# Kernel tuning notes

Measured on AMD Instinct MI355X. Metric: run time of the kernel, lower is better.

Reference implementation:

```python
import jax, jax.numpy as jnp
import numpy as np

STATE_DIM, ACTION_DIM, HIDDEN_DIM = 512, 64, 2048
INPUT_DIM = STATE_DIM + ACTION_DIM + 1  # 577
BATCH = 4096


def setup_inputs() -> dict:
    key = jax.random.key(0)
    ks = jax.random.split(key, 12)
    sc_x = 1.0 / np.sqrt(INPUT_DIM)
    sc_h = 1.0 / np.sqrt(HIDDEN_DIM)
    return {
        "s": jax.random.normal(ks[0], (BATCH, STATE_DIM), jnp.float32),
        "a_prev": jax.random.normal(ks[1], (BATCH, ACTION_DIM), jnp.float32),
        "r_prev": jax.random.normal(ks[2], (BATCH, 1), jnp.float32),
        "h": jnp.zeros((HIDDEN_DIM,), jnp.float32),
        "c": jnp.zeros((HIDDEN_DIM,), jnp.float32),
        # Fused gate weights: columns ordered [i, f, g(c-tilde), o]
        "Wx": jax.random.uniform(ks[3], (INPUT_DIM, 4 * HIDDEN_DIM), jnp.float32, -sc_x, sc_x),
        "Wh": jax.random.uniform(ks[4], (HIDDEN_DIM, 4 * HIDDEN_DIM), jnp.float32, -sc_h, sc_h),
        "bh": jax.random.uniform(ks[5], (4 * HIDDEN_DIM,), jnp.float32, -sc_h, sc_h),
        "Wa": jax.random.uniform(ks[6], (HIDDEN_DIM, ACTION_DIM), jnp.float32, -sc_h, sc_h),
        "ba": jax.random.uniform(ks[7], (ACTION_DIM,), jnp.float32, -sc_h, sc_h),
        "Wv": jax.random.uniform(ks[8], (HIDDEN_DIM, 1), jnp.float32, -sc_h, sc_h),
        "bv": jax.random.uniform(ks[9], (1,), jnp.float32, -sc_h, sc_h),
    }


def reference(s, a_prev, r_prev, h, c, Wx, Wh, bh, Wa, ba, Wv, bv):
    # x: [B, input_dim]
    x = jnp.concatenate([s, a_prev, r_prev], axis=1)
    # Two fused GEMMs replace the 8 separate small linears (same math).
    z = x @ Wx + h @ Wh + bh          # [B, 4H]
    zi, zf, zg, zo = jnp.split(z, 4, axis=-1)
    i = jax.nn.sigmoid(zi)
    f = jax.nn.sigmoid(zf)
    c_new = f * c + i * jnp.tanh(zg)  # [B, H] (c broadcast over batch)
    o = jax.nn.sigmoid(zo)
    h_new = o * jnp.tanh(c_new)       # [B, H]
    probs = jax.nn.softmax(h_new @ Wa + ba, axis=1)  # [B, A]
    v = h_new @ Wv + bv               # [B, 1]
    return (probs, v)
```

## Files before the change

kernel.cpp:

```cpp
#include <hip/hip_runtime.h>
#include <hip/hip_bf16.h>

#define BATCH   4096
#define SDIM    512
#define ADIM    64
#define IDIM    577
#define KP2     576
#define NKT64   9
#define HDIM    2048
#define ZDIM    8192
#define BUFE    (128 * 64)

typedef __attribute__((ext_vector_type(8))) __bf16 bf16x8;
typedef __attribute__((ext_vector_type(4))) __bf16 bf16x4;
typedef __attribute__((ext_vector_type(4))) float  accx4;

__global__ __launch_bounds__(256) void setup_kernel(
    const float* __restrict__ s, const float* __restrict__ a_prev,
    const float* __restrict__ h,
    const float* __restrict__ wx, const float* __restrict__ wh,
    const float* __restrict__ wa,
    __hip_bfloat16* __restrict__ xb, __hip_bfloat16* __restrict__ wxt,
    __hip_bfloat16* __restrict__ waT, float* __restrict__ zh_w)
{
    __shared__ float stile[64 * 65];
    const int bid = blockIdx.x;
    const int t = threadIdx.x;

    if (bid < 1152) {
        const int kt2 = bid >> 7;
        const int nt  = bid & 127;
        const int c4  = t & 15;
        const int rr  = t >> 4;
#pragma unroll
        for (int i = 0; i < 4; ++i) {
            const int r = rr + i * 16;
            const int k = kt2 * 64 + r;
            float4 v =
                *(const float4*)(wx + (size_t)k * ZDIM + nt * 64 + c4 * 4);
            *(float4*)(stile + r * 65 + c4 * 4) = v;
        }
        __syncthreads();
        const int ch = t & 7;
#pragma unroll
        for (int i = 0; i < 2; ++i) {
            const int nr = (t >> 3) + i * 32;
            bf16x8 w8;
#pragma unroll
            for (int j = 0; j < 8; ++j)
                w8[j] = (__bf16)stile[(ch * 8 + j) * 65 + nr];
            *(bf16x8*)(wxt + (size_t)(nt * 64 + nr) * KP2 + kt2 * 64 + ch * 8)
                = w8;
        }
    } else if (bid < 2176) {
        const int zb = bid - 1152;
        const int nb = zb & 63, ky = zb >> 6;
        const int n  = nb * 128 + (t & 127);
        const int kh = t >> 7;
        const float* hp  = h + ky * 128 + kh * 64;
        const float* whp = wh + (size_t)(ky * 128 + kh * 64) * ZDIM + n;
        float p = 0.0f;
#pragma unroll 32
        for (int kk = 0; kk < 64; ++kk)
            p = fmaf(hp[kk], whp[(size_t)kk * ZDIM], p);
        stile[t] = p;
        __syncthreads();
        if (t < 128)
            zh_w[ky * ZDIM + n] = stile[t] + stile[t + 128];
    } else if (bid < 2432) {
        const int row0 = (bid - 2176) * 16;
        const int tr = t >> 4, tc = t & 15;
        const int row = row0 + tr;
        const float* srow = s + (size_t)row * SDIM;
        const float* arow = a_prev + (size_t)row * ADIM;
        __hip_bfloat16* xrow = xb + (size_t)row * KP2;
#pragma unroll
        for (int j = 0; j < 9; ++j) {
            const int c4  = j * 16 + tc;
            const int col = c4 * 4;
            float4 v = (col < SDIM)
                ? *(const float4*)(srow + col)
                : *(const float4*)(arow + (col - SDIM));
            bf16x4 w;
            w[0] = (__bf16)v.x; w[1] = (__bf16)v.y;
            w[2] = (__bf16)v.z; w[3] = (__bf16)v.w;
            *(bf16x4*)(xrow + col) = w;
        }
    } else {
        const int wb = bid - 2432;
        const int kt = wb >> 1, at = wb & 1;
        const int c  = t & 31, r0 = t >> 5;
#pragma unroll
        for (int i = 0; i < 4; ++i) {
            int r = r0 + i * 8;
            stile[r * 33 + c] = wa[(size_t)(kt * 32 + r) * ADIM + at * 32 + c];
        }
        __syncthreads();
#pragma unroll
        for (int i = 0; i < 4; ++i) {
            int r = r0 + i * 8;
            waT[(size_t)(at * 32 + r) * HDIM + kt * 32 + c] =
                __float2bfloat16(stile[c * 33 + r]);
        }
    }
}

__device__ __forceinline__ float rcp_f(float x) {
    return __builtin_amdgcn_rcpf(x);
}
__device__ __forceinline__ float sigmoid_f(float x) {
    return rcp_f(1.0f + __expf(-x));
}
__device__ __forceinline__ float tanh_f(float x) {
    return 1.0f - 2.0f * rcp_f(1.0f + __expf(2.0f * x));
}

__global__ __launch_bounds__(256, 4) void lstm_gemm(
    const __hip_bfloat16* __restrict__ xb,
    const __hip_bfloat16* __restrict__ wxt,
    const float* __restrict__ zh_w,
    const float* __restrict__ bh,
    const float* __restrict__ cvec,
    const float* __restrict__ wx,
    const float* __restrict__ r_prev,
    __hip_bfloat16* __restrict__ hout)
{
    __shared__ __bf16 smA[BUFE];
    __shared__ __bf16 smB[BUFE];
    const int t    = threadIdx.x;
    const int lane = t & 63;
    const int wid  = t >> 6;
    const int m0   = blockIdx.x * 128;
    const int n0   = blockIdx.y * 32;
    const int wm   = wid >> 1, wn = wid & 1;
    const int fl15 = lane & 15;
    const int fhi  = lane >> 4;

    accx4 acc[4][4] = {};

    const int srow = lane >> 3;
    const int slot = lane & 7;
    const int cch  = slot ^ srow;
    const __bf16* gA[4]; const __bf16* gB[4]; int lofs[4];
#pragma unroll
    for (int i = 0; i < 4; ++i) {
        const int r = wid * 32 + i * 8 + srow;
        gA[i] = (const __bf16*)xb + (size_t)(m0 + r) * KP2 + cch * 8;
        const int g = r >> 5, nn = r & 31;
        gB[i] = (const __bf16*)wxt +
                (size_t)(g * HDIM + n0 + nn) * KP2 + cch * 8;
        lofs[i] = (wid * 32 + i * 8) * 64;
    }

    auto stage = [&](int tile) {
        const int ko = tile * 64;
#pragma unroll
        for (int i = 0; i < 4; ++i) {
            __builtin_amdgcn_global_load_lds(
                (const __attribute__((address_space(1))) void*)(gA[i] + ko),
                (__attribute__((address_space(3))) void*)(smA + lofs[i]),
                16, 0, 0);
            __builtin_amdgcn_global_load_lds(
                (const __attribute__((address_space(1))) void*)(gB[i] + ko),
                (__attribute__((address_space(3))) void*)(smB + lofs[i]),
                16, 0, 0);
        }
    };

    auto compute = [&]() {
#pragma unroll
        for (int hf = 0; hf < 2; ++hf) {
            const int ck = hf * 4 + fhi;
            const int sl = (ck ^ (fl15 & 7)) * 8;
            bf16x8 af[4], bfr[4];
#pragma unroll
            for (int rt = 0; rt < 4; ++rt)
                af[rt] = *(const bf16x8*)(smA +
                    (wm * 64 + rt * 16 + fl15) * 64 + sl);
#pragma unroll
            for (int g = 0; g < 4; ++g)
                bfr[g] = *(const bf16x8*)(smB +
                    (g * 32 + wn * 16 + fl15) * 64 + sl);
#pragma unroll
            for (int g = 0; g < 4; ++g)
#pragma unroll
                for (int rt = 0; rt < 4; ++rt)
                    acc[g][rt] = __builtin_amdgcn_mfma_f32_16x16x32_bf16(
                        af[rt], bfr[g], acc[g][rt], 0, 0, 0);
        }
    };

#pragma unroll
    for (int kt = 0; kt < NKT64; ++kt) {
        if (kt) __syncthreads();
        stage(kt);
        __syncthreads();
        compute();
    }

    const int colg = n0 + wn * 16 + fl15;
    float zsum[4], wxr[4];
#pragma unroll
    for (int g = 0; g < 4; ++g) {
        float z = bh[g * HDIM + colg];
#pragma unroll
        for (int j = 0; j < 16; ++j)
            z += zh_w[j * ZDIM + g * HDIM + colg];
        zsum[g] = z;
        wxr[g] = wx[(size_t)576 * ZDIM + g * HDIM + colg];
    }
    const float cv = cvec[colg];
#pragma unroll
    for (int rt = 0; rt < 4; ++rt) {
#pragma unroll
        for (int r = 0; r < 4; ++r) {
            const int row = m0 + wm * 64 + rt * 16 + (fhi << 2) + r;
            const float rv = r_prev[row];
            const float zi = acc[0][rt][r] + zsum[0] + rv * wxr[0];
            const float zf = acc[1][rt][r] + zsum[1] + rv * wxr[1];
            const float zg = acc[2][rt][r] + zsum[2] + rv * wxr[2];
            const float zo = acc[3][rt][r] + zsum[3] + rv * wxr[3];
            const float cn = sigmoid_f(zf) * cv + sigmoid_f(zi) * tanh_f(zg);
            const float hn = sigmoid_f(zo) * tanh_f(cn);
            hout[(size_t)row * HDIM + colg] = __float2bfloat16(hn);
        }
    }
}

__global__ __launch_bounds__(512) void head_kernel(
    const __hip_bfloat16* __restrict__ hnew,
    const __hip_bfloat16* __restrict__ waT,
    const float* __restrict__ wv,
    const float* __restrict__ ba, const float* __restrict__ bv,
    float* __restrict__ probs, float* __restrict__ vout)
{
    __shared__ float lg[8][16][68];
    __shared__ float vpart[8][16];
    const int t    = threadIdx.x;
    const int lane = t & 63;
    const int w    = t >> 6;
    const int r0   = blockIdx.x * 16;
    const int fl15 = lane & 15, fhi = lane >> 4;
    const int k0   = w * 256;

    const __bf16* arow = (const __bf16*)hnew +
        (size_t)(r0 + fl15) * HDIM + k0 + fhi * 8;
    const __bf16* brow = (const __bf16*)waT +
        (size_t)fl15 * HDIM + k0 + fhi * 8;
    const float* wvp = wv + k0 + fhi * 8;

    accx4 acc[4] = {};
    float va0 = 0.f, va1 = 0.f;
#pragma unroll
    for (int kk = 0; kk < 256; kk += 32) {
        bf16x8 af = *(const bf16x8*)(arow + kk);
#pragma unroll
        for (int a = 0; a < 4; ++a) {
            bf16x8 bf = *(const bf16x8*)(brow + (size_t)a * 16 * HDIM + kk);
            acc[a] = __builtin_amdgcn_mfma_f32_16x16x32_bf16(
                af, bf, acc[a], 0, 0, 0);
        }
#pragma unroll
        for (int j = 0; j < 4; ++j) {
            va0 = fmaf((float)af[j],     wvp[kk + j],     va0);
            va1 = fmaf((float)af[j + 4], wvp[kk + j + 4], va1);
        }
    }
#pragma unroll
    for (int a = 0; a < 4; ++a)
#pragma unroll
        for (int r = 0; r < 4; ++r)
            lg[w][fhi * 4 + r][a * 16 + fl15] = acc[a][r];
    float va = va0 + va1;
    va += __shfl_xor(va, 16);
    va += __shfl_xor(va, 32);
    if (lane < 16) vpart[w][lane] = va;
    __syncthreads();

    const float bav = ba[lane];
#pragma unroll
    for (int i = 0; i < 2; ++i) {
        const int row = w * 2 + i;
        float logit = bav;
#pragma unroll
        for (int p = 0; p < 8; ++p)
            logit += lg[p][row][lane];
        float m = logit;
#pragma unroll
        for (int mask = 32; mask >= 1; mask >>= 1)
            m = fmaxf(m, __shfl_xor(m, mask));
        const float e = __expf(logit - m);
        float ssum = e;
#pragma unroll
        for (int mask = 32; mask >= 1; mask >>= 1)
            ssum += __shfl_xor(ssum, mask);
        probs[(size_t)(r0 + row) * 64 + lane] = e / ssum;
    }
    if (t < 16) {
        float v = bv[0];
#pragma unroll
        for (int p = 0; p < 8; ++p)
            v += vpart[p][t];
        vout[r0 + t] = v;
    }
}

extern "C" void kernel_launch(void* const* d_in, const int* in_sizes, int n_in,
                              void* d_out, int out_size, void* d_ws,
                              size_t ws_size, hipStream_t stream)
{
    const float* s      = (const float*)d_in[0];
    const float* a_prev = (const float*)d_in[1];
    const float* r_prev = (const float*)d_in[2];
    const float* h      = (const float*)d_in[3];
    const float* c      = (const float*)d_in[4];
    const float* Wx     = (const float*)d_in[5];
    const float* Wh     = (const float*)d_in[6];
    const float* bh     = (const float*)d_in[7];
    const float* Wa     = (const float*)d_in[8];
    const float* ba     = (const float*)d_in[9];
    const float* Wv     = (const float*)d_in[10];
    const float* bv     = (const float*)d_in[11];

    float* out   = (float*)d_out;
    float* probs = out;
    float* vout  = out + (size_t)BATCH * ADIM;

    char* ws = (char*)d_ws;
    __hip_bfloat16* xb   = (__hip_bfloat16*)ws;
    __hip_bfloat16* wxt  = (__hip_bfloat16*)(ws + 4718592);
    __hip_bfloat16* waT  = (__hip_bfloat16*)(ws + 14155776);
    float* zh_w          = (float*)(ws + 14417920);
    __hip_bfloat16* hnew = (__hip_bfloat16*)(ws + 14942208);

    setup_kernel<<<2560, 256, 0, stream>>>(
        s, a_prev, h, Wx, Wh, Wa, xb, wxt, waT, zh_w);
    lstm_gemm<<<dim3(BATCH / 128, HDIM / 32), 256, 0, stream>>>(
        xb, wxt, zh_w, bh, c, Wx, r_prev, hnew);
    head_kernel<<<BATCH / 16, 512, 0, stream>>>(
        hnew, waT, Wv, ba, bv, probs, vout);
}
```

Before: 219.8 us.

## Widen LSTM GEMM tile to 64 columns and triple-buffer LDS loads

The gate GEMM block grows to 512 threads covering 128 rows by 64 hidden columns across all four gates, so each A tile is shared by twice as many columns. Global-to-LDS staging becomes a three-stage ring: tiles are prefetched two ahead, and explicit vmcnt waits with raw barriers replace the two __syncthreads per K step. This targets load latency and barrier stalls, but raises LDS use to 144 KB per block, and the hand-written waitcnt counts must match the exact number of issued loads.

```diff
diff --git a/kernel.cpp b/kernel.cpp
--- a/kernel.cpp
+++ b/kernel.cpp
@@ -9,7 +9,8 @@
 #define NKT64   9
 #define HDIM    2048
 #define ZDIM    8192
-#define BUFE    (128 * 64)
+#define AELEM   (128 * 64)
+#define BELEM   (256 * 64)
 
 typedef __attribute__((ext_vector_type(8))) __bf16 bf16x8;
 typedef __attribute__((ext_vector_type(4))) __bf16 bf16x4;
@@ -115,7 +116,7 @@
     return 1.0f - 2.0f * rcp_f(1.0f + __expf(2.0f * x));
 }
 
-__global__ __launch_bounds__(256, 4) void lstm_gemm(
+__global__ __launch_bounds__(512, 2) void lstm_gemm(
     const __hip_bfloat16* __restrict__ xb,
     const __hip_bfloat16* __restrict__ wxt,
     const float* __restrict__ zh_w,
@@ -125,14 +126,15 @@
     const float* __restrict__ r_prev,
     __hip_bfloat16* __restrict__ hout)
 {
-    __shared__ __bf16 smA[BUFE];
-    __shared__ __bf16 smB[BUFE];
+    __shared__ __bf16 smA[3 * AELEM];
+    __shared__ __bf16 smB[3 * BELEM];
     const int t    = threadIdx.x;
     const int lane = t & 63;
     const int wid  = t >> 6;
     const int m0   = blockIdx.x * 128;
-    const int n0   = blockIdx.y * 32;
-    const int wm   = wid >> 1, wn = wid & 1;
+    const int n0   = blockIdx.y * 64;
+    const int wm   = wid >> 2;
+    const int wn   = wid & 3;
     const int fl15 = lane & 15;
     const int fhi  = lane >> 4;
 
@@ -141,33 +143,43 @@
     const int srow = lane >> 3;
     const int slot = lane & 7;
     const int cch  = slot ^ srow;
-    const __bf16* gA[4]; const __bf16* gB[4]; int lofs[4];
+    const __bf16* gA[2]; int lofsA[2];
+    const __bf16* gB[4]; int lofsB[4];
+#pragma unroll
+    for (int i = 0; i < 2; ++i) {
+        const int rA = wid * 16 + i * 8 + srow;
+        gA[i] = (const __bf16*)xb + (size_t)(m0 + rA) * KP2 + cch * 8;
+        lofsA[i] = (wid * 16 + i * 8) * 64;
+    }
 #pragma unroll
     for (int i = 0; i < 4; ++i) {
-        const int r = wid * 32 + i * 8 + srow;
-        gA[i] = (const __bf16*)xb + (size_t)(m0 + r) * KP2 + cch * 8;
-        const int g = r >> 5, nn = r & 31;
+        const int rB = wid * 32 + i * 8 + srow;
+        const int g = rB >> 6, c = rB & 63;
         gB[i] = (const __bf16*)wxt +
-                (size_t)(g * HDIM + n0 + nn) * KP2 + cch * 8;
-        lofs[i] = (wid * 32 + i * 8) * 64;
-    }
-
-    auto stage = [&](int tile) {
+                (size_t)(g * HDIM + n0 + c) * KP2 + cch * 8;
+        lofsB[i] = (wid * 32 + i * 8) * 64;
+    }
+
+    auto stage = [&](int tile, int buf) {
         const int ko = tile * 64;
 #pragma unroll
-        for (int i = 0; i < 4; ++i) {
+        for (int i = 0; i < 2; ++i)
             __builtin_amdgcn_global_load_lds(
                 (const __attribute__((address_space(1))) void*)(gA[i] + ko),
-                (__attribute__((address_space(3))) void*)(smA + lofs[i]),
+                (__attribute__((address_space(3))) void*)(smA + buf * AELEM +
+                                                          lofsA[i]),
                 16, 0, 0);
+#pragma unroll
+        for (int i = 0; i < 4; ++i)
             __builtin_amdgcn_global_load_lds(
                 (const __attribute__((address_space(1))) void*)(gB[i] + ko),
-                (__attribute__((address_space(3))) void*)(smB + lofs[i]),
+                (__attribute__((address_space(3))) void*)(smB + buf * BELEM +
+                                                          lofsB[i]),
                 16, 0, 0);
-        }
     };
 
-    auto compute = [&]() {
+    auto compute = [&](int buf) {
+        const int poA = buf * AELEM, poB = buf * BELEM;
 #pragma unroll
         for (int hf = 0; hf < 2; ++hf) {
             const int ck = hf * 4 + fhi;
@@ -175,12 +187,12 @@
             bf16x8 af[4], bfr[4];
 #pragma unroll
             for (int rt = 0; rt < 4; ++rt)
-                af[rt] = *(const bf16x8*)(smA +
+                af[rt] = *(const bf16x8*)(smA + poA +
                     (wm * 64 + rt * 16 + fl15) * 64 + sl);
 #pragma unroll
             for (int g = 0; g < 4; ++g)
-                bfr[g] = *(const bf16x8*)(smB +
-                    (g * 32 + wn * 16 + fl15) * 64 + sl);
+                bfr[g] = *(const bf16x8*)(smB + poB +
+                    (g * 64 + wn * 16 + fl15) * 64 + sl);
 #pragma unroll
             for (int g = 0; g < 4; ++g)
 #pragma unroll
@@ -190,12 +202,20 @@
         }
     };
 
+    stage(0, 0);
+    stage(1, 1);
 #pragma unroll
     for (int kt = 0; kt < NKT64; ++kt) {
-        if (kt) __syncthreads();
-        stage(kt);
-        __syncthreads();
-        compute();
+        asm volatile("s_barrier" ::: "memory");
+        if (kt + 2 < NKT64) stage(kt + 2, (kt + 2) % 3);
+        if (kt < NKT64 - 2)
+            asm volatile("s_waitcnt vmcnt(12)" ::: "memory");
+        else if (kt == NKT64 - 2)
+            asm volatile("s_waitcnt vmcnt(6)" ::: "memory");
+        else
+            asm volatile("s_waitcnt vmcnt(0)" ::: "memory");
+        asm volatile("s_barrier" ::: "memory");
+        compute(kt % 3);
     }
 
     const int colg = n0 + wn * 16 + fl15;
@@ -335,7 +355,7 @@
 
     setup_kernel<<<2560, 256, 0, stream>>>(
         s, a_prev, h, Wx, Wh, Wa, xb, wxt, waT, zh_w);
-    lstm_gemm<<<dim3(BATCH / 128, HDIM / 32), 256, 0, stream>>>(
+    lstm_gemm<<<dim3(BATCH / 128, HDIM / 64), 512, 0, stream>>>(
         xb, wxt, zh_w, bh, c, Wx, r_prev, hnew);
     head_kernel<<<BATCH / 16, 512, 0, stream>>>(
         hnew, waT, Wv, ba, bv, probs, vout);
```

Result: faster. 210.6 us (-4.2%).

## Enlarge LSTM GEMM tile to 256x256 with double-buffered LDS and phased prefetch

Applied to the files above, without the earlier changes.

The fused LSTM gate GEMM moves from 128x128 tiles on 256 threads to 256x256 tiles on 512 threads, so each wave holds more accumulators and reuses each LDS fragment more often. LDS is double-buffered: the next K-tile is staged via global_load_lds in two halves interleaved with the MFMA phases, and setprio is raised around the MFMA bursts. This targets the exposed global-load latency and the per-tile syncthreads stalls of the single-buffer loop. The grid shrinks to 512 blocks, and the larger LDS footprint and register use lower occupancy.

```diff
diff --git a/kernel.cpp b/kernel.cpp
--- a/kernel.cpp
+++ b/kernel.cpp
@@ -9,7 +9,7 @@
 #define NKT64   9
 #define HDIM    2048
 #define ZDIM    8192
-#define BUFE    (128 * 64)
+#define TELEM   (256 * 64)
 
 typedef __attribute__((ext_vector_type(8))) __bf16 bf16x8;
 typedef __attribute__((ext_vector_type(4))) __bf16 bf16x4;
@@ -115,7 +115,7 @@
     return 1.0f - 2.0f * rcp_f(1.0f + __expf(2.0f * x));
 }
 
-__global__ __launch_bounds__(256, 4) void lstm_gemm(
+__global__ __launch_bounds__(512, 2) void lstm_gemm(
     const __hip_bfloat16* __restrict__ xb,
     const __hip_bfloat16* __restrict__ wxt,
     const float* __restrict__ zh_w,
@@ -125,18 +125,19 @@
     const float* __restrict__ r_prev,
     __hip_bfloat16* __restrict__ hout)
 {
-    __shared__ __bf16 smA[BUFE];
-    __shared__ __bf16 smB[BUFE];
+    __shared__ __bf16 smA[2 * TELEM];
+    __shared__ __bf16 smB[2 * TELEM];
     const int t    = threadIdx.x;
     const int lane = t & 63;
     const int wid  = t >> 6;
-    const int m0   = blockIdx.x * 128;
-    const int n0   = blockIdx.y * 32;
-    const int wm   = wid >> 1, wn = wid & 1;
+    const int m0   = blockIdx.x * 256;
+    const int n0h  = blockIdx.y * 64;
+    const int wm   = wid >> 2;
+    const int wn   = wid & 3;
     const int fl15 = lane & 15;
     const int fhi  = lane >> 4;
 
-    accx4 acc[4][4] = {};
+    accx4 acc[4][8] = {};
 
     const int srow = lane >> 3;
     const int slot = lane & 7;
@@ -144,61 +145,82 @@
     const __bf16* gA[4]; const __bf16* gB[4]; int lofs[4];
 #pragma unroll
     for (int i = 0; i < 4; ++i) {
-        const int r = wid * 32 + i * 8 + srow;
-        gA[i] = (const __bf16*)xb + (size_t)(m0 + r) * KP2 + cch * 8;
-        const int g = r >> 5, nn = r & 31;
-        gB[i] = (const __bf16*)wxt +
-                (size_t)(g * HDIM + n0 + nn) * KP2 + cch * 8;
+        const int rA = wid * 32 + i * 8 + srow;
+        gA[i] = (const __bf16*)xb + (size_t)(m0 + rA) * KP2 + cch * 8;
+        const int b  = wid * 32 + i * 8 + srow;
+        const int zb = ((b >> 4) & 3) * HDIM + n0h + (b >> 6) * 16 + (b & 15);
+        gB[i] = (const __bf16*)wxt + (size_t)zb * KP2 + cch * 8;
         lofs[i] = (wid * 32 + i * 8) * 64;
     }
 
-    auto stage = [&](int tile) {
+    auto stage_half = [&](int tile, int bufp, int half) {
         const int ko = tile * 64;
-#pragma unroll
-        for (int i = 0; i < 4; ++i) {
+        const int po = bufp * TELEM;
+#pragma unroll
+        for (int i = half * 2; i < half * 2 + 2; ++i) {
             __builtin_amdgcn_global_load_lds(
                 (const __attribute__((address_space(1))) void*)(gA[i] + ko),
-                (__attribute__((address_space(3))) void*)(smA + lofs[i]),
+                (__attribute__((address_space(3))) void*)(smA + po + lofs[i]),
                 16, 0, 0);
             __builtin_amdgcn_global_load_lds(
                 (const __attribute__((address_space(1))) void*)(gB[i] + ko),
-                (__attribute__((address_space(3))) void*)(smB + lofs[i]),
+                (__attribute__((address_space(3))) void*)(smB + po + lofs[i]),
                 16, 0, 0);
         }
     };
 
-    auto compute = [&]() {
-#pragma unroll
-        for (int hf = 0; hf < 2; ++hf) {
-            const int ck = hf * 4 + fhi;
-            const int sl = (ck ^ (fl15 & 7)) * 8;
-            bf16x8 af[4], bfr[4];
-#pragma unroll
-            for (int rt = 0; rt < 4; ++rt)
-                af[rt] = *(const bf16x8*)(smA +
-                    (wm * 64 + rt * 16 + fl15) * 64 + sl);
+    stage_half(0, 0, 0);
+    stage_half(0, 0, 1);
+
+#pragma unroll
+    for (int kt = 0; kt < NKT64; ++kt) {
+        const int p  = kt & 1;
+        const int po = p * TELEM;
+        asm volatile("s_waitcnt vmcnt(0)" ::: "memory");
+        __builtin_amdgcn_s_barrier();
+        bf16x8 bfr[4][2];
+#pragma unroll
+        for (int ph = 0; ph < 4; ++ph) {
+            if (kt + 1 < NKT64 && ph < 2)
+                stage_half(kt + 1, (kt + 1) & 1, ph);
+            bf16x8 af[2][2];
+            if (ph == 0) {
+#pragma unroll
+                for (int g = 0; g < 4; ++g)
+#pragma unroll
+                    for (int hf = 0; hf < 2; ++hf) {
+                        const int sl = ((hf * 4 + fhi) ^ (fl15 & 7)) * 8;
+                        bfr[g][hf] = *(const bf16x8*)(smB + po +
+                            (wn * 64 + g * 16 + fl15) * 64 + sl);
+                    }
+            }
+#pragma unroll
+            for (int rs = 0; rs < 2; ++rs)
+#pragma unroll
+                for (int hf = 0; hf < 2; ++hf) {
+                    const int sl = ((hf * 4 + fhi) ^ (fl15 & 7)) * 8;
+                    af[rs][hf] = *(const bf16x8*)(smA + po +
+                        (wm * 128 + (ph * 2 + rs) * 16 + fl15) * 64 + sl);
+                }
+            __builtin_amdgcn_s_barrier();
+            asm volatile("s_waitcnt lgkmcnt(0)" ::: "memory");
+            __builtin_amdgcn_sched_barrier(0);
+            __builtin_amdgcn_s_setprio(1);
 #pragma unroll
             for (int g = 0; g < 4; ++g)
-                bfr[g] = *(const bf16x8*)(smB +
-                    (g * 32 + wn * 16 + fl15) * 64 + sl);
-#pragma unroll
-            for (int g = 0; g < 4; ++g)
-#pragma unroll
-                for (int rt = 0; rt < 4; ++rt)
-                    acc[g][rt] = __builtin_amdgcn_mfma_f32_16x16x32_bf16(
-                        af[rt], bfr[g], acc[g][rt], 0, 0, 0);
-        }
-    };
-
-#pragma unroll
-    for (int kt = 0; kt < NKT64; ++kt) {
-        if (kt) __syncthreads();
-        stage(kt);
-        __syncthreads();
-        compute();
-    }
-
-    const int colg = n0 + wn * 16 + fl15;
+#pragma unroll
+                for (int rs = 0; rs < 2; ++rs)
+#pragma unroll
+                    for (int hf = 0; hf < 2; ++hf)
+                        acc[g][ph * 2 + rs] =
+                            __builtin_amdgcn_mfma_f32_16x16x32_bf16(
+                                af[rs][hf], bfr[g][hf], acc[g][ph * 2 + rs],
+                                0, 0, 0);
+            __builtin_amdgcn_s_setprio(0);
+        }
+    }
+
+    const int colg = n0h + wn * 16 + fl15;
     float zsum[4], wxr[4];
 #pragma unroll
     for (int g = 0; g < 4; ++g) {
@@ -211,10 +233,10 @@
     }
     const float cv = cvec[colg];
 #pragma unroll
-    for (int rt = 0; rt < 4; ++rt) {
+    for (int rt = 0; rt < 8; ++rt) {
 #pragma unroll
         for (int r = 0; r < 4; ++r) {
-            const int row = m0 + wm * 64 + rt * 16 + (fhi << 2) + r;
+            const int row = m0 + wm * 128 + rt * 16 + (fhi << 2) + r;
             const float rv = r_prev[row];
             const float zi = acc[0][rt][r] + zsum[0] + rv * wxr[0];
             const float zf = acc[1][rt][r] + zsum[1] + rv * wxr[1];
@@ -335,7 +357,7 @@
 
     setup_kernel<<<2560, 256, 0, stream>>>(
         s, a_prev, h, Wx, Wh, Wa, xb, wxt, waT, zh_w);
-    lstm_gemm<<<dim3(BATCH / 128, HDIM / 32), 256, 0, stream>>>(
+    lstm_gemm<<<dim3(BATCH / 256, HDIM / 64), 512, 0, stream>>>(
         xb, wxt, zh_w, bh, c, Wx, r_prev, hnew);
     head_kernel<<<BATCH / 16, 512, 0, stream>>>(
         hnew, waT, Wv, ba, bv, probs, vout);
```

Result: faster. 206.4 us (-6.1%).
